# Kernel optimization log

Measured on AMD Instinct MI355X. Metric: run time of the kernel, lower is better.

## Reference

```python
import jax, jax.numpy as jnp
import numpy as np

N = 100000
E = 1600000
D = 64
EPS = 1e-5


def setup_inputs() -> dict:
    key = jax.random.key(0)
    ks = jax.random.split(key, 16)
    edge_index = jax.random.randint(ks[0], (2, E), 0, N, dtype=jnp.int64)
    node_attr = jax.random.normal(ks[1], (N, D), dtype=jnp.float32)
    edge_attr = jax.random.normal(ks[2], (E, D), dtype=jnp.float32)
    scale = 1.0 / np.sqrt(D)
    params = {}
    for i, k in enumerate(range(3, 3 + 3)):
        li = i + 1
        kw, kb = jax.random.split(ks[k])
        params[f"W{li}"] = jax.random.uniform(kw, (D, D), jnp.float32, -scale, scale)
        params[f"b{li}"] = jax.random.uniform(kb, (D,), jnp.float32, -scale, scale)
        params[f"gamma{li}"] = jnp.ones((D,), jnp.float32)
        params[f"beta{li}"] = jnp.zeros((D,), jnp.float32)
    return {"edge_index": edge_index, "node_attr": node_attr, "edge_attr": edge_attr, **params}


def _gcn_conv(x, src, dst, dinv, W, b):
    # GCNConv: h = D^{-1/2} (A + I) D^{-1/2} (x W) + b  (symmetric norm, self-loops)
    h = x @ W  # [N, D]
    norm = (dinv[src] * dinv[dst])[:, None]  # [E, 1]
    agg = jax.ops.segment_sum(h[src] * norm, dst, num_segments=N)  # neighbor messages
    agg = agg + (dinv * dinv)[:, None] * h  # self-loop contribution
    return agg + b


def _bn(x, gamma, beta):
    # BatchNorm1d in training mode: batch statistics over the node dimension
    mean = jnp.mean(x, axis=0)
    var = jnp.var(x, axis=0)
    return gamma * (x - mean) * jax.lax.rsqrt(var + EPS) + beta


def reference(edge_index, node_attr, edge_attr,
              W1, b1, gamma1, beta1,
              W2, b2, gamma2, beta2,
              W3, b3, gamma3, beta3):
    src, dst = edge_index[0], edge_index[1]
    # degree including self-loop (PyG gcn_norm: deg computed at target + 1)
    deg = jnp.zeros((N,), jnp.float32).at[dst].add(1.0) + 1.0
    dinv = jax.lax.rsqrt(deg)
    x = _bn(jax.nn.relu(_gcn_conv(node_attr, src, dst, dinv, W1, b1)), gamma1, beta1)
    x = _bn(jax.nn.relu(_gcn_conv(x, src, dst, dinv, W2, b2)), gamma2, beta2)
    x = _bn(jax.nn.relu(_gcn_conv(x, src, dst, dinv, W3, b3)), gamma3, beta3)
    return x
```

## Files before the change

kernel.cpp:

```cpp
#include <hip/hip_runtime.h>

#define N_NODES 100000
#define N_EDGES 1600000
#define D 64
#define EPS 1e-5f


#define SCAN_BLOCKS 128
#define SCAN_T 256

__global__ void setup_kernel(const unsigned* __restrict__ ei, int* __restrict__ flag,
                             int* __restrict__ deg, float* __restrict__ stats) {
    int t = blockIdx.x * 256 + threadIdx.x;
    if (t < N_NODES) deg[t] = 0;
    if (t < 384) stats[t] = 0.f;
    if (blockIdx.x == gridDim.x - 1) {
        int tt = threadIdx.x;
        unsigned stride = (2u * (unsigned)N_EDGES) / 256u;
        unsigned v = ei[(unsigned)tt * stride + 1u];
        __shared__ unsigned red[256];
        red[tt] = v;
        __syncthreads();
        for (int s = 128; s > 0; s >>= 1) {
            if (tt < s) red[tt] |= red[tt + s];
            __syncthreads();
        }
        if (tt == 0) *flag = (red[0] == 0u) ? 1 : 0;
    }
}

__device__ __forceinline__ int load_idx(const void* ei, int is64, size_t pos) {
    if (is64) return (int)((const long long*)ei)[pos];
    return ((const int*)ei)[pos];
}

__global__ void degcount_kernel(const void* __restrict__ ei, const int* __restrict__ flag,
                                int* __restrict__ deg) {
    int e = blockIdx.x * 256 + threadIdx.x;
    if (e >= N_EDGES) return;
    int is64 = *flag;
    int d = load_idx(ei, is64, (size_t)N_EDGES + e);
    atomicAdd(&deg[d], 1);
}

__global__ void scanA_kernel(const int* __restrict__ deg, float* __restrict__ dinv,
                             int* __restrict__ bsum) {
    int b = blockIdx.x, t = threadIdx.x;
    const int chunk = (N_NODES + SCAN_BLOCKS - 1) / SCAN_BLOCKS;
    const int tchunk = (chunk + SCAN_T - 1) / SCAN_T;
    int lo = b * chunk + t * tchunk;
    int hi = min(lo + tchunk, min((b + 1) * chunk, N_NODES));
    int s = 0;
    for (int i = lo; i < hi; ++i) {
        int d = deg[i];
        s += d;
        dinv[i] = rsqrtf((float)d + 1.0f);
    }
    __shared__ int red[SCAN_T];
    red[t] = s;
    __syncthreads();
    for (int st = 128; st > 0; st >>= 1) {
        if (t < st) red[t] += red[t + st];
        __syncthreads();
    }
    if (t == 0) bsum[b] = red[0];
}

__global__ void scanB_kernel(int* __restrict__ bsum) {
    __shared__ int sh[SCAN_BLOCKS];
    int t = threadIdx.x;
    sh[t] = bsum[t];
    __syncthreads();
    for (int st = 1; st < SCAN_BLOCKS; st <<= 1) {
        int v = (t >= st) ? sh[t - st] : 0;
        __syncthreads();
        sh[t] += v;
        __syncthreads();
    }
    bsum[t] = (t == 0) ? 0 : sh[t - 1];
}

__global__ void scanC_kernel(const int* __restrict__ deg, const int* __restrict__ bsum,
                             int* __restrict__ off, int* __restrict__ cursor) {
    int b = blockIdx.x, t = threadIdx.x;
    const int chunk = (N_NODES + SCAN_BLOCKS - 1) / SCAN_BLOCKS;
    const int tchunk = (chunk + SCAN_T - 1) / SCAN_T;
    int lo = b * chunk + t * tchunk;
    int hi = min(lo + tchunk, min((b + 1) * chunk, N_NODES));
    int s = 0;
    for (int i = lo; i < hi; ++i) s += deg[i];
    __shared__ int red[SCAN_T];
    red[t] = s;
    __syncthreads();
    for (int st = 1; st < SCAN_T; st <<= 1) {
        int v = (t >= st) ? red[t - st] : 0;
        __syncthreads();
        red[t] += v;
        __syncthreads();
    }
    int tbase = bsum[b] + red[t] - s;
    for (int i = lo; i < hi; ++i) {
        int d = deg[i];
        off[i] = tbase;
        cursor[i] = tbase;
        tbase += d;
    }
    if (b == 0 && t == 0) off[N_NODES] = N_EDGES;
}

__global__ void bucket_kernel(const void* __restrict__ ei, const int* __restrict__ flag,
                              const float* __restrict__ dinv, int* __restrict__ cursor,
                              long long* __restrict__ packed) {
    int e = blockIdx.x * 256 + threadIdx.x;
    if (e >= N_EDGES) return;
    int is64 = *flag;
    int s = load_idx(ei, is64, e);
    int d = load_idx(ei, is64, (size_t)N_EDGES + e);
    int pos = atomicAdd(&cursor[d], 1);
    unsigned long long pk =
        (unsigned long long)(unsigned)s |
        ((unsigned long long)__float_as_uint(dinv[s]) << 32);
    __builtin_nontemporal_store((long long)pk, &packed[pos]);
}

__global__ __launch_bounds__(256) void gemm_kernel(const float* __restrict__ x,
                                                   const float* __restrict__ W,
                                                   float* __restrict__ h) {
    int lane = threadIdx.x & 63;
    int wv = threadIdx.x >> 6;
    float wcol[64];
#pragma unroll
    for (int k = 0; k < 64; ++k) wcol[k] = W[k * 64 + lane];
    int row0 = blockIdx.x * 64;
    for (int r = wv; r < 64; r += 4) {
        int row = row0 + r;
        if (row >= N_NODES) break;
        const float* xr = x + (size_t)row * 64;
        float acc = 0.f;
#pragma unroll
        for (int k = 0; k < 64; ++k) acc += xr[k] * wcol[k];
        h[(size_t)row * 64 + lane] = acc;
    }
}

__global__ __launch_bounds__(256) void gather_kernel(const float* __restrict__ h,
                                                     const int* __restrict__ off,
                                                     const long long* __restrict__ packed,
                                                     const float* __restrict__ dinv,
                                                     const float* __restrict__ b,
                                                     float* __restrict__ agg) {
    int lane = threadIdx.x & 63;
    int wv = threadIdx.x >> 6;
    int n = blockIdx.x * 4 + wv;
    if (n >= N_NODES) return;
    int g = lane >> 4;
    int fq = lane & 15;
    float dn = dinv[n];
    float4 acc = make_float4(0.f, 0.f, 0.f, 0.f);
    int j0 = off[n], j1 = off[n + 1];
    for (int j = j0; j < j1; j += 4) {
        int jj = j + g;
        if (jj < j1) {
            long long pk = packed[jj];
            int s = (int)(pk & 0xffffffffLL);
            float w = __int_as_float((int)(pk >> 32)) * dn;
            float4 hv = reinterpret_cast<const float4*>(h + (size_t)s * 64)[fq];
            acc.x += w * hv.x;
            acc.y += w * hv.y;
            acc.z += w * hv.z;
            acc.w += w * hv.w;
        }
    }
#pragma unroll
    for (int m = 16; m <= 32; m <<= 1) {
        acc.x += __shfl_xor(acc.x, m, 64);
        acc.y += __shfl_xor(acc.y, m, 64);
        acc.z += __shfl_xor(acc.z, m, 64);
        acc.w += __shfl_xor(acc.w, m, 64);
    }
    if (g == 0) {
        float4 hv = reinterpret_cast<const float4*>(h + (size_t)n * 64)[fq];
        float4 bv = reinterpret_cast<const float4*>(b)[fq];
        float sw = dn * dn;
        float4 o;
        o.x = acc.x + sw * hv.x + bv.x;
        o.y = acc.y + sw * hv.y + bv.y;
        o.z = acc.z + sw * hv.z + bv.z;
        o.w = acc.w + sw * hv.w + bv.w;
        reinterpret_cast<float4*>(agg + (size_t)n * 64)[fq] = o;
    }
}

__global__ __launch_bounds__(256) void stats_kernel(const float* __restrict__ agg,
                                                    float* __restrict__ stats) {
    int lane = threadIdx.x & 63;
    int sub = threadIdx.x >> 6;
    float s1 = 0.f, s2 = 0.f;
    for (int r = blockIdx.x * 4 + sub; r < N_NODES; r += gridDim.x * 4) {
        float v = agg[(size_t)r * 64 + lane];
        v = fmaxf(v, 0.f);
        s1 += v;
        s2 += v * v;
    }
    __shared__ float red[2][4][64];
    red[0][sub][lane] = s1;
    red[1][sub][lane] = s2;
    __syncthreads();
    if (sub == 0) {
        s1 = red[0][0][lane] + red[0][1][lane] + red[0][2][lane] + red[0][3][lane];
        s2 = red[1][0][lane] + red[1][1][lane] + red[1][2][lane] + red[1][3][lane];
        atomicAdd(&stats[lane], s1);
        atomicAdd(&stats[64 + lane], s2);
    }
}

__global__ __launch_bounds__(256) void apply_kernel(const float* __restrict__ agg,
                                                    const float* __restrict__ stats,
                                                    const float* __restrict__ gamma,
                                                    const float* __restrict__ beta,
                                                    float* __restrict__ out) {
    int i = blockIdx.x * 256 + threadIdx.x;
    if (i >= N_NODES * 16) return;
    int d0 = (i & 15) << 2;
    float4 v = reinterpret_cast<const float4*>(agg)[i];
    float r[4] = {v.x, v.y, v.z, v.w};
    float4 o;
    float* op = &o.x;
    const float invN = 1.0f / (float)N_NODES;
#pragma unroll
    for (int j = 0; j < 4; ++j) {
        int d = d0 + j;
        float mean = stats[d] * invN;
        float var = stats[64 + d] * invN - mean * mean;
        float rs = rsqrtf(var + EPS);
        float val = fmaxf(r[j], 0.f);
        op[j] = gamma[d] * (val - mean) * rs + beta[d];
    }
    reinterpret_cast<float4*>(out)[i] = o;
}

extern "C" void kernel_launch(void* const* d_in, const int* in_sizes, int n_in,
                              void* d_out, int out_size, void* d_ws, size_t ws_size,
                              hipStream_t stream) {
    const void* ei = d_in[0];
    const float* node_attr = (const float*)d_in[1];

    char* ws = (char*)d_ws;
    int* flag = (int*)(ws + 0);
    int* deg = (int*)(ws + 256);
    float* dinv = (float*)(ws + 400256);
    int* off = (int*)(ws + 800256);
    int* bsum = (int*)(ws + 1200384);
    int* cursor = (int*)(ws + 1200896);
    float* stats = (float*)(ws + 1600896);
    long long* packed = (long long*)(ws + 1602432);
    float* h = (float*)(ws + 14402432);
    float* agg = (float*)(ws + 40002432);
    float* xbuf = (float*)(ws + 65602432);

    setup_kernel<<<(N_NODES + 255) / 256, 256, 0, stream>>>((const unsigned*)ei, flag, deg, stats);
    degcount_kernel<<<N_EDGES / 256, 256, 0, stream>>>(ei, flag, deg);
    scanA_kernel<<<SCAN_BLOCKS, SCAN_T, 0, stream>>>(deg, dinv, bsum);
    scanB_kernel<<<1, SCAN_BLOCKS, 0, stream>>>(bsum);
    scanC_kernel<<<SCAN_BLOCKS, SCAN_T, 0, stream>>>(deg, bsum, off, cursor);
    bucket_kernel<<<N_EDGES / 256, 256, 0, stream>>>(ei, flag, dinv, cursor, packed);

    const float* x = node_attr;
    for (int l = 0; l < 3; ++l) {
        const float* W = (const float*)d_in[3 + 4 * l];
        const float* b = (const float*)d_in[4 + 4 * l];
        const float* gamma = (const float*)d_in[5 + 4 * l];
        const float* beta = (const float*)d_in[6 + 4 * l];
        float* stats_l = stats + 128 * l;

        gemm_kernel<<<(N_NODES + 63) / 64, 256, 0, stream>>>(x, W, h);
        gather_kernel<<<(N_NODES + 3) / 4, 256, 0, stream>>>(h, off, packed, dinv, b, agg);
        stats_kernel<<<1024, 256, 0, stream>>>(agg, stats_l);
        float* outp = (l == 2) ? (float*)d_out : xbuf;
        apply_kernel<<<(N_NODES * 16 + 255) / 256, 256, 0, stream>>>(agg, stats_l, gamma, beta, outp);
        x = xbuf;
    }
}
```

Measured before the change: 1.169 ms.

## Fold BatchNorm into next layer's weights and vectorize edge/GEMM/stats kernels

Folds each layer's BatchNorm affine transform into the next layer's GEMM by scaling W rows and adding a bias vector (prep_kernel). This removes the intermediate apply pass for layers 1 and 2, saving a full read and write of the node features each time. ReLU moves into the gather epilogue, and the stats kernel is vectorized to float4 with shuffle reductions. Edge preprocessing now handles two edges per thread, the GEMM uses float4 loads with split accumulators, and the gather is unrolled by two with separate accumulators. The risk is a small floating-point reassociation from the folded weights, plus one extra tiny launch per layer.

After: 1.188 ms. About the same (+1.6%).

```diff
diff --git a/kernel.cpp b/kernel.cpp
--- a/kernel.cpp
+++ b/kernel.cpp
@@ -10,10 +10,12 @@
 #define SCAN_T 256
 
 __global__ void setup_kernel(const unsigned* __restrict__ ei, int* __restrict__ flag,
-                             int* __restrict__ deg, float* __restrict__ stats) {
+                             int* __restrict__ deg, float* __restrict__ stats,
+                             float* __restrict__ c0) {
     int t = blockIdx.x * 256 + threadIdx.x;
     if (t < N_NODES) deg[t] = 0;
     if (t < 384) stats[t] = 0.f;
+    if (t < 64) c0[t] = 0.f;
     if (blockIdx.x == gridDim.x - 1) {
         int tt = threadIdx.x;
         unsigned stride = (2u * (unsigned)N_EDGES) / 256u;
@@ -29,18 +31,22 @@
     }
 }
 
-__device__ __forceinline__ int load_idx(const void* ei, int is64, size_t pos) {
-    if (is64) return (int)((const long long*)ei)[pos];
-    return ((const int*)ei)[pos];
-}
-
 __global__ void degcount_kernel(const void* __restrict__ ei, const int* __restrict__ flag,
                                 int* __restrict__ deg) {
-    int e = blockIdx.x * 256 + threadIdx.x;
-    if (e >= N_EDGES) return;
-    int is64 = *flag;
-    int d = load_idx(ei, is64, (size_t)N_EDGES + e);
-    atomicAdd(&deg[d], 1);
+    int t = blockIdx.x * 256 + threadIdx.x;
+    if (t >= N_EDGES / 2) return;
+    int d0, d1;
+    if (*flag) {
+        const longlong2* dp = (const longlong2*)((const long long*)ei + N_EDGES);
+        longlong2 d = dp[t];
+        d0 = (int)d.x; d1 = (int)d.y;
+    } else {
+        const int2* dp = (const int2*)((const int*)ei + N_EDGES);
+        int2 d = dp[t];
+        d0 = d.x; d1 = d.y;
+    }
+    atomicAdd(&deg[d0], 1);
+    atomicAdd(&deg[d1], 1);
 }
 
 __global__ void scanA_kernel(const int* __restrict__ deg, float* __restrict__ dinv,
@@ -111,35 +117,55 @@
 __global__ void bucket_kernel(const void* __restrict__ ei, const int* __restrict__ flag,
                               const float* __restrict__ dinv, int* __restrict__ cursor,
                               long long* __restrict__ packed) {
-    int e = blockIdx.x * 256 + threadIdx.x;
-    if (e >= N_EDGES) return;
-    int is64 = *flag;
-    int s = load_idx(ei, is64, e);
-    int d = load_idx(ei, is64, (size_t)N_EDGES + e);
-    int pos = atomicAdd(&cursor[d], 1);
-    unsigned long long pk =
-        (unsigned long long)(unsigned)s |
-        ((unsigned long long)__float_as_uint(dinv[s]) << 32);
-    __builtin_nontemporal_store((long long)pk, &packed[pos]);
+    int t = blockIdx.x * 256 + threadIdx.x;
+    if (t >= N_EDGES / 2) return;
+    int s0, s1, d0, d1;
+    if (*flag) {
+        const longlong2* sp = (const longlong2*)ei;
+        const longlong2* dp = (const longlong2*)((const long long*)ei + N_EDGES);
+        longlong2 s = sp[t], d = dp[t];
+        s0 = (int)s.x; s1 = (int)s.y; d0 = (int)d.x; d1 = (int)d.y;
+    } else {
+        const int2* sp = (const int2*)ei;
+        const int2* dp = (const int2*)((const int*)ei + N_EDGES);
+        int2 s = sp[t], d = dp[t];
+        s0 = s.x; s1 = s.y; d0 = d.x; d1 = d.y;
+    }
+    int p0 = atomicAdd(&cursor[d0], 1);
+    int p1 = atomicAdd(&cursor[d1], 1);
+    unsigned long long pk0 = (unsigned long long)(unsigned)s0 |
+                             ((unsigned long long)__float_as_uint(dinv[s0]) << 32);
+    unsigned long long pk1 = (unsigned long long)(unsigned)s1 |
+                             ((unsigned long long)__float_as_uint(dinv[s1]) << 32);
+    __builtin_nontemporal_store((long long)pk0, &packed[p0]);
+    __builtin_nontemporal_store((long long)pk1, &packed[p1]);
 }
 
 __global__ __launch_bounds__(256) void gemm_kernel(const float* __restrict__ x,
                                                    const float* __restrict__ W,
+                                                   const float* __restrict__ c,
                                                    float* __restrict__ h) {
     int lane = threadIdx.x & 63;
     int wv = threadIdx.x >> 6;
     float wcol[64];
 #pragma unroll
     for (int k = 0; k < 64; ++k) wcol[k] = W[k * 64 + lane];
+    float bias = c[lane];
     int row0 = blockIdx.x * 64;
     for (int r = wv; r < 64; r += 4) {
         int row = row0 + r;
         if (row >= N_NODES) break;
-        const float* xr = x + (size_t)row * 64;
-        float acc = 0.f;
-#pragma unroll
-        for (int k = 0; k < 64; ++k) acc += xr[k] * wcol[k];
-        h[(size_t)row * 64 + lane] = acc;
+        const float4* xr = reinterpret_cast<const float4*>(x + (size_t)row * 64);
+        float a0 = 0.f, a1 = 0.f, a2 = 0.f, a3 = 0.f;
+#pragma unroll
+        for (int k4 = 0; k4 < 16; ++k4) {
+            float4 xv = xr[k4];
+            a0 += xv.x * wcol[4 * k4 + 0];
+            a1 += xv.y * wcol[4 * k4 + 1];
+            a2 += xv.z * wcol[4 * k4 + 2];
+            a3 += xv.w * wcol[4 * k4 + 3];
+        }
+        h[(size_t)row * 64 + lane] = (a0 + a1) + (a2 + a3) + bias;
     }
 }
 
@@ -155,38 +181,51 @@
     if (n >= N_NODES) return;
     int g = lane >> 4;
     int fq = lane & 15;
+    const float4* h4 = reinterpret_cast<const float4*>(h);
     float dn = dinv[n];
-    float4 acc = make_float4(0.f, 0.f, 0.f, 0.f);
+    float4 acc0 = make_float4(0.f, 0.f, 0.f, 0.f);
+    float4 acc1 = make_float4(0.f, 0.f, 0.f, 0.f);
     int j0 = off[n], j1 = off[n + 1];
-    for (int j = j0; j < j1; j += 4) {
+    int j = j0;
+    for (; j + 8 <= j1; j += 8) {
+        long long pk0 = packed[j + g];
+        long long pk1 = packed[j + 4 + g];
+        int s0 = (int)(pk0 & 0xffffffffLL);
+        int s1 = (int)(pk1 & 0xffffffffLL);
+        float w0 = __int_as_float((int)(pk0 >> 32)) * dn;
+        float w1 = __int_as_float((int)(pk1 >> 32)) * dn;
+        float4 h0 = h4[s0 * 16 + fq];
+        float4 h1 = h4[s1 * 16 + fq];
+        acc0.x += w0 * h0.x; acc0.y += w0 * h0.y; acc0.z += w0 * h0.z; acc0.w += w0 * h0.w;
+        acc1.x += w1 * h1.x; acc1.y += w1 * h1.y; acc1.z += w1 * h1.z; acc1.w += w1 * h1.w;
+    }
+    for (; j < j1; j += 4) {
         int jj = j + g;
         if (jj < j1) {
             long long pk = packed[jj];
             int s = (int)(pk & 0xffffffffLL);
             float w = __int_as_float((int)(pk >> 32)) * dn;
-            float4 hv = reinterpret_cast<const float4*>(h + (size_t)s * 64)[fq];
-            acc.x += w * hv.x;
-            acc.y += w * hv.y;
-            acc.z += w * hv.z;
-            acc.w += w * hv.w;
+            float4 hv = h4[s * 16 + fq];
+            acc0.x += w * hv.x; acc0.y += w * hv.y; acc0.z += w * hv.z; acc0.w += w * hv.w;
         }
     }
+    acc0.x += acc1.x; acc0.y += acc1.y; acc0.z += acc1.z; acc0.w += acc1.w;
 #pragma unroll
     for (int m = 16; m <= 32; m <<= 1) {
-        acc.x += __shfl_xor(acc.x, m, 64);
-        acc.y += __shfl_xor(acc.y, m, 64);
-        acc.z += __shfl_xor(acc.z, m, 64);
-        acc.w += __shfl_xor(acc.w, m, 64);
+        acc0.x += __shfl_xor(acc0.x, m, 64);
+        acc0.y += __shfl_xor(acc0.y, m, 64);
+        acc0.z += __shfl_xor(acc0.z, m, 64);
+        acc0.w += __shfl_xor(acc0.w, m, 64);
     }
     if (g == 0) {
-        float4 hv = reinterpret_cast<const float4*>(h + (size_t)n * 64)[fq];
+        float4 hv = h4[n * 16 + fq];
         float4 bv = reinterpret_cast<const float4*>(b)[fq];
         float sw = dn * dn;
         float4 o;
-        o.x = acc.x + sw * hv.x + bv.x;
-        o.y = acc.y + sw * hv.y + bv.y;
-        o.z = acc.z + sw * hv.z + bv.z;
-        o.w = acc.w + sw * hv.w + bv.w;
+        o.x = fmaxf(acc0.x + sw * hv.x + bv.x, 0.f);
+        o.y = fmaxf(acc0.y + sw * hv.y + bv.y, 0.f);
+        o.z = fmaxf(acc0.z + sw * hv.z + bv.z, 0.f);
+        o.w = fmaxf(acc0.w + sw * hv.w + bv.w, 0.f);
         reinterpret_cast<float4*>(agg + (size_t)n * 64)[fq] = o;
     }
 }
@@ -195,22 +234,55 @@
                                                     float* __restrict__ stats) {
     int lane = threadIdx.x & 63;
     int sub = threadIdx.x >> 6;
-    float s1 = 0.f, s2 = 0.f;
-    for (int r = blockIdx.x * 4 + sub; r < N_NODES; r += gridDim.x * 4) {
-        float v = agg[(size_t)r * 64 + lane];
-        v = fmaxf(v, 0.f);
-        s1 += v;
-        s2 += v * v;
-    }
-    __shared__ float red[2][4][64];
-    red[0][sub][lane] = s1;
-    red[1][sub][lane] = s2;
-    __syncthreads();
-    if (sub == 0) {
-        s1 = red[0][0][lane] + red[0][1][lane] + red[0][2][lane] + red[0][3][lane];
-        s2 = red[1][0][lane] + red[1][1][lane] + red[1][2][lane] + red[1][3][lane];
-        atomicAdd(&stats[lane], s1);
-        atomicAdd(&stats[64 + lane], s2);
+    int fq = lane & 15, rs = lane >> 4;
+    const float4* a4 = reinterpret_cast<const float4*>(agg);
+    float4 s1 = make_float4(0.f, 0.f, 0.f, 0.f);
+    float4 s2 = make_float4(0.f, 0.f, 0.f, 0.f);
+    for (int r4 = blockIdx.x * 4 + sub; r4 < N_NODES / 4; r4 += gridDim.x * 4) {
+        float4 v = a4[(size_t)(r4 * 4 + rs) * 16 + fq];
+        s1.x += v.x; s1.y += v.y; s1.z += v.z; s1.w += v.w;
+        s2.x += v.x * v.x; s2.y += v.y * v.y; s2.z += v.z * v.z; s2.w += v.w * v.w;
+    }
+#pragma unroll
+    for (int m = 16; m <= 32; m <<= 1) {
+        s1.x += __shfl_xor(s1.x, m, 64); s1.y += __shfl_xor(s1.y, m, 64);
+        s1.z += __shfl_xor(s1.z, m, 64); s1.w += __shfl_xor(s1.w, m, 64);
+        s2.x += __shfl_xor(s2.x, m, 64); s2.y += __shfl_xor(s2.y, m, 64);
+        s2.z += __shfl_xor(s2.z, m, 64); s2.w += __shfl_xor(s2.w, m, 64);
+    }
+    __shared__ float red[4][128];
+    if (rs == 0) {
+        reinterpret_cast<float4*>(&red[sub][0])[fq] = s1;
+        reinterpret_cast<float4*>(&red[sub][64])[fq] = s2;
+    }
+    __syncthreads();
+    int t = threadIdx.x;
+    if (t < 128) {
+        float v = red[0][t] + red[1][t] + red[2][t] + red[3][t];
+        atomicAdd(&stats[t], v);
+    }
+}
+
+__global__ void prep_kernel(const float* __restrict__ stats, const float* __restrict__ gamma,
+                            const float* __restrict__ beta, const float* __restrict__ W,
+                            float* __restrict__ Weff, float* __restrict__ ceff) {
+    __shared__ float s_scale[64], s_shift[64];
+    int t = threadIdx.x;
+    if (t < 64) {
+        const float invN = 1.0f / (float)N_NODES;
+        float mean = stats[t] * invN;
+        float var = stats[64 + t] * invN - mean * mean;
+        float rs = rsqrtf(var + EPS);
+        float sc = gamma[t] * rs;
+        s_scale[t] = sc;
+        s_shift[t] = beta[t] - sc * mean;
+    }
+    __syncthreads();
+    for (int idx = t; idx < 4096; idx += 256) Weff[idx] = s_scale[idx >> 6] * W[idx];
+    if (t < 64) {
+        float c = 0.f;
+        for (int k = 0; k < 64; ++k) c += s_shift[k] * W[k * 64 + t];
+        ceff[t] = c;
     }
 }
 
@@ -233,8 +305,7 @@
         float mean = stats[d] * invN;
         float var = stats[64 + d] * invN - mean * mean;
         float rs = rsqrtf(var + EPS);
-        float val = fmaxf(r[j], 0.f);
-        op[j] = gamma[d] * (val - mean) * rs + beta[d];
+        op[j] = gamma[d] * (r[j] - mean) * rs + beta[d];
     }
     reinterpret_cast<float4*>(out)[i] = o;
 }
@@ -253,31 +324,48 @@
     int* bsum = (int*)(ws + 1200384);
     int* cursor = (int*)(ws + 1200896);
     float* stats = (float*)(ws + 1600896);
-    long long* packed = (long long*)(ws + 1602432);
-    float* h = (float*)(ws + 14402432);
-    float* agg = (float*)(ws + 40002432);
-    float* xbuf = (float*)(ws + 65602432);
-
-    setup_kernel<<<(N_NODES + 255) / 256, 256, 0, stream>>>((const unsigned*)ei, flag, deg, stats);
-    degcount_kernel<<<N_EDGES / 256, 256, 0, stream>>>(ei, flag, deg);
+    float* c0 = (float*)(ws + 1602432);
+    float* Weff = (float*)(ws + 1602688);
+    float* ceff = (float*)(ws + 1619072);
+    long long* packed = (long long*)(ws + 1619456);
+    float* h = (float*)(ws + 14419456);
+    float* agg = (float*)(ws + 40019456);
+
+    setup_kernel<<<(N_NODES + 255) / 256, 256, 0, stream>>>((const unsigned*)ei, flag, deg,
+                                                            stats, c0);
+    degcount_kernel<<<(N_EDGES / 2 + 255) / 256, 256, 0, stream>>>(ei, flag, deg);
     scanA_kernel<<<SCAN_BLOCKS, SCAN_T, 0, stream>>>(deg, dinv, bsum);
     scanB_kernel<<<1, SCAN_BLOCKS, 0, stream>>>(bsum);
     scanC_kernel<<<SCAN_BLOCKS, SCAN_T, 0, stream>>>(deg, bsum, off, cursor);
-    bucket_kernel<<<N_EDGES / 256, 256, 0, stream>>>(ei, flag, dinv, cursor, packed);
+    bucket_kernel<<<(N_EDGES / 2 + 255) / 256, 256, 0, stream>>>(ei, flag, dinv, cursor, packed);
 
     const float* x = node_attr;
     for (int l = 0; l < 3; ++l) {
         const float* W = (const float*)d_in[3 + 4 * l];
         const float* b = (const float*)d_in[4 + 4 * l];
-        const float* gamma = (const float*)d_in[5 + 4 * l];
-        const float* beta = (const float*)d_in[6 + 4 * l];
         float* stats_l = stats + 128 * l;
 
-        gemm_kernel<<<(N_NODES + 63) / 64, 256, 0, stream>>>(x, W, h);
+        const float* Wuse;
+        const float* cuse;
+        if (l == 0) {
+            Wuse = W;
+            cuse = c0;
+        } else {
+            const float* gamma_p = (const float*)d_in[5 + 4 * (l - 1)];
+            const float* beta_p = (const float*)d_in[6 + 4 * (l - 1)];
+            prep_kernel<<<1, 256, 0, stream>>>(stats + 128 * (l - 1), gamma_p, beta_p, W,
+                                               Weff, ceff);
+            Wuse = Weff;
+            cuse = ceff;
+        }
+
+        gemm_kernel<<<(N_NODES + 63) / 64, 256, 0, stream>>>(x, Wuse, cuse, h);
         gather_kernel<<<(N_NODES + 3) / 4, 256, 0, stream>>>(h, off, packed, dinv, b, agg);
         stats_kernel<<<1024, 256, 0, stream>>>(agg, stats_l);
-        float* outp = (l == 2) ? (float*)d_out : xbuf;
-        apply_kernel<<<(N_NODES * 16 + 255) / 256, 256, 0, stream>>>(agg, stats_l, gamma, beta, outp);
-        x = xbuf;
-    }
-}
+        x = agg;
+    }
+    const float* gamma3 = (const float*)d_in[5 + 4 * 2];
+    const float* beta3 = (const float*)d_in[6 + 4 * 2];
+    apply_kernel<<<(N_NODES * 16 + 255) / 256, 256, 0, stream>>>(agg, stats + 256, gamma3,
+                                                                 beta3, (float*)d_out);
+}
```
